# Optimization experiments

Measured on AMD Instinct MI355X. Metric: run time of the kernel, lower is better.

## Reference

```python
import jax, jax.numpy as jnp
import numpy as np

DIM_CAP = 16   # capsule dim
NCLS = 17      # annotation_nr
BS = 16
T = 120        # chunk_size * fps
P = 22         # players per frame graph
G = BS * T     # number of graphs = 1920
N = G * P      # nodes = 42240
C_IN = 14
CHS = [16, 32, 64, 152]  # 8m,16m,32m,76m with m=2
BN_EPS = 1e-3


def _build_graph():
    # fully-connected directed edges within each 22-node graph (no self loops)
    ii, jj = np.meshgrid(np.arange(P), np.arange(P), indexing='ij')
    mask = ii != jj
    li, lj = ii[mask], jj[mask]               # (462,)
    base = (np.arange(G) * P)[:, None]
    src = (base + li[None, :]).reshape(-1)
    dst = (base + lj[None, :]).reshape(-1)
    edge_index = np.stack([src, dst]).astype(np.int64)   # (2, E)
    batch = np.repeat(np.arange(G), P).astype(np.int64)  # (N,)
    return jnp.asarray(edge_index), jnp.asarray(batch)


def setup_inputs() -> dict:
    key = jax.random.key(0)
    ks = jax.random.split(key, 16)
    edge_index, batch = _build_graph()
    E = edge_index.shape[1]
    x = jax.random.normal(ks[0], (N, C_IN), dtype=jnp.float32)
    edge_attr = jax.random.uniform(ks[1], (E, 5), dtype=jnp.float32)
    dims = [C_IN] + CHS
    params = {}
    for i in range(4):
        s = 1.0 / np.sqrt(dims[i])
        params[f'W{i+1}'] = jax.random.normal(ks[2 + i], (dims[i], dims[i + 1]), dtype=jnp.float32) * s
        params[f'b{i+1}'] = jnp.zeros((dims[i + 1],), dtype=jnp.float32)
    c_out = DIM_CAP * NCLS  # 272
    params['conv_w'] = jax.random.normal(ks[6], (c_out, CHS[-1], 3), dtype=jnp.float32) * (1.0 / np.sqrt(CHS[-1] * 3))
    params['conv_b'] = jnp.zeros((c_out,), dtype=jnp.float32)
    params['bn_gamma'] = jnp.ones((T,), dtype=jnp.float32)
    params['bn_beta'] = jnp.zeros((T,), dtype=jnp.float32)
    return dict(x=x, edge_index=edge_index, batch=batch, edge_attr=edge_attr, **params)


def _gcn_layer(x, src, dst, w_edge, W, b):
    # PyG GCNConv: x' = D^-1/2 (A + I) D^-1/2 (x W) + b, edge weights w, self-loop weight 1
    n = x.shape[0]
    h = x @ W
    loop = jnp.arange(n)
    src_f = jnp.concatenate([src, loop])
    dst_f = jnp.concatenate([dst, loop])
    w_f = jnp.concatenate([w_edge, jnp.ones((n,), h.dtype)])
    deg = jax.ops.segment_sum(w_f, dst_f, num_segments=n)
    dinv = jnp.where(deg > 0, jax.lax.rsqrt(deg), 0.0)
    norm = dinv[src_f] * w_f * dinv[dst_f]
    out = jax.ops.segment_sum(norm[:, None] * h[src_f], dst_f, num_segments=n)
    return out + b


def reference(x, edge_index, batch, edge_attr, W1, b1, W2, b2, W3, b3, W4, b4,
              conv_w, conv_b, bn_gamma, bn_beta):
    src, dst = edge_index[0], edge_index[1]
    ew = edge_attr[:, 4]
    h = jax.nn.relu(_gcn_layer(x, src, dst, ew, W1, b1))
    h = jax.nn.relu(_gcn_layer(h, src, dst, ew, W2, b2))
    h = jax.nn.relu(_gcn_layer(h, src, dst, ew, W3, b3))
    h = jax.nn.relu(_gcn_layer(h, src, dst, ew, W4, b4))
    # global mean pool per graph -> (G, 152)
    ones = jnp.ones((h.shape[0],), h.dtype)
    cnt = jax.ops.segment_sum(ones, batch, num_segments=G)
    pooled = jax.ops.segment_sum(h, batch, num_segments=G) / jnp.clip(cnt, 1.0)[:, None]
    # (BS, T, 152) -> (BS, 152, T); conv kernel (3,1) with pad (1,1) on T
    feat = pooled.reshape(BS, T, CHS[-1]).transpose(0, 2, 1)
    conv = jax.lax.conv_general_dilated(
        feat, conv_w, window_strides=(1,), padding=[(1, 1)],
        dimension_numbers=('NCH', 'OIH', 'NCH'))
    conv = conv + conv_b[None, :, None]            # (BS, 272, T)
    caps = conv.transpose(0, 2, 1).reshape(BS, T, DIM_CAP, NCLS)
    # BatchNorm2d(num_features=T) in eval mode: running mean 0, var 1
    scale = (bn_gamma / jnp.sqrt(1.0 + BN_EPS))[None, :, None, None]
    shift = bn_beta[None, :, None, None]
    s = jax.nn.sigmoid(caps * scale + shift)
    out = jnp.sqrt(jnp.sum(jnp.square(s - 0.5), axis=2) * 4.0 / DIM_CAP)
    return out  # (BS, T, NCLS)
```

## Files before the change

### kernel.cpp

```cpp
#include <hip/hip_runtime.h>
#include <hip/hip_bf16.h>

#define GROUPS 1920
#define CH4 152

__device__ __forceinline__ int rh(int r) { return (r + (r >> 3)) & 7; }
__device__ __forceinline__ int swz(int r, int c) {
    return (r << 5) + ((((c >> 2) ^ rh(r)) << 2) | (c & 3));
}
__device__ __forceinline__ int swz4(int r, int c4) {
    return (r << 5) + ((c4 ^ rh(r)) << 2);
}

template<int DIN, int KR>
__device__ __forceinline__ void layerA(const float* buf, float* Ut,
                                       const float* A, int tid)
{
    constexpr int NT = (DIN / KR) * 3;
    if (tid < NT) {
        const int kt = tid / 3, pt = tid - kt * 3;
        const int p0 = pt * 8;
        float acc[KR][8];
        #pragma unroll
        for (int j = 0; j < KR; ++j)
            #pragma unroll
            for (int a = 0; a < 8; ++a) acc[j][a] = 0.f;
        #pragma unroll 2
        for (int q = 0; q < 22; ++q) {
            const float4 a0 = *(const float4*)(A + q * 28 + p0);
            const float4 a1 = *(const float4*)(A + q * 28 + p0 + 4);
            float xv[KR];
            #pragma unroll
            for (int j = 0; j < KR; ++j) xv[j] = buf[swz(kt * KR + j, q)];
            #pragma unroll
            for (int j = 0; j < KR; ++j) {
                acc[j][0] = fmaf(xv[j], a0.x, acc[j][0]);
                acc[j][1] = fmaf(xv[j], a0.y, acc[j][1]);
                acc[j][2] = fmaf(xv[j], a0.z, acc[j][2]);
                acc[j][3] = fmaf(xv[j], a0.w, acc[j][3]);
                acc[j][4] = fmaf(xv[j], a1.x, acc[j][4]);
                acc[j][5] = fmaf(xv[j], a1.y, acc[j][5]);
                acc[j][6] = fmaf(xv[j], a1.z, acc[j][6]);
                acc[j][7] = fmaf(xv[j], a1.w, acc[j][7]);
            }
        }
        #pragma unroll
        for (int j = 0; j < KR; ++j) {
            const int k = kt * KR + j;
            *(float4*)(Ut + swz4(k, pt * 2)) =
                make_float4(acc[j][0], acc[j][1], acc[j][2], acc[j][3]);
            *(float4*)(Ut + swz4(k, pt * 2 + 1)) =
                make_float4(acc[j][4], acc[j][5], acc[j][6], acc[j][7]);
        }
    }
}

template<int DIN, int DOUT, int CR>
__device__ __forceinline__ void layerB(const float* __restrict__ W,
                                       const float* __restrict__ Bb,
                                       const float* Ut, float* buf, int tid)
{
    constexpr int NT = (DOUT / CR) * 3;
    if (tid < NT) {
        const int ct = tid / 3, pt = tid - ct * 3;
        const int c0 = ct * CR;
        float acc[CR][8];
        #pragma unroll
        for (int b = 0; b < CR; ++b) {
            const float bias = Bb[c0 + b];
            #pragma unroll
            for (int a = 0; a < 8; ++a) acc[b][a] = bias;
        }
        #pragma unroll 2
        for (int k = 0; k < DIN; ++k) {
            const float4 u0 = *(const float4*)(Ut + swz4(k, pt * 2));
            const float4 u1 = *(const float4*)(Ut + swz4(k, pt * 2 + 1));
            float wv[CR];
            if constexpr (CR == 1) {
                wv[0] = W[k * DOUT + c0];
            } else if constexpr (CR == 2) {
                const float2 w2 = *(const float2*)(W + k * DOUT + c0);
                wv[0] = w2.x; wv[1] = w2.y;
            } else {
                #pragma unroll
                for (int b = 0; b < CR; b += 4) {
                    const float4 w4 = *(const float4*)(W + k * DOUT + c0 + b);
                    wv[b] = w4.x; wv[b + 1] = w4.y; wv[b + 2] = w4.z; wv[b + 3] = w4.w;
                }
            }
            #pragma unroll
            for (int b = 0; b < CR; ++b) {
                acc[b][0] = fmaf(wv[b], u0.x, acc[b][0]);
                acc[b][1] = fmaf(wv[b], u0.y, acc[b][1]);
                acc[b][2] = fmaf(wv[b], u0.z, acc[b][2]);
                acc[b][3] = fmaf(wv[b], u0.w, acc[b][3]);
                acc[b][4] = fmaf(wv[b], u1.x, acc[b][4]);
                acc[b][5] = fmaf(wv[b], u1.y, acc[b][5]);
                acc[b][6] = fmaf(wv[b], u1.z, acc[b][6]);
                acc[b][7] = fmaf(wv[b], u1.w, acc[b][7]);
            }
        }
        #pragma unroll
        for (int b = 0; b < CR; ++b) {
            const int r = c0 + b;
            *(float4*)(buf + swz4(r, pt * 2)) =
                make_float4(fmaxf(acc[b][0], 0.f), fmaxf(acc[b][1], 0.f),
                            fmaxf(acc[b][2], 0.f), fmaxf(acc[b][3], 0.f));
            *(float4*)(buf + swz4(r, pt * 2 + 1)) =
                make_float4(fmaxf(acc[b][4], 0.f), fmaxf(acc[b][5], 0.f),
                            fmaxf(acc[b][6], 0.f), fmaxf(acc[b][7], 0.f));
        }
    }
}

__global__ __launch_bounds__(64) void gcn_kernel(
    const float* __restrict__ x, const float* __restrict__ ea,
    const float* __restrict__ W1, const float* __restrict__ b1,
    const float* __restrict__ W2, const float* __restrict__ b2,
    const float* __restrict__ W3, const float* __restrict__ b3,
    const float* __restrict__ W4, const float* __restrict__ b4,
    float* __restrict__ pooledT)
{
    __shared__ __align__(16) float sA[24 * 28];
    __shared__ float dv[24];
    __shared__ __align__(16) float buf[64 * 32];
    __shared__ __align__(16) float Ut[64 * 32];

    const int tid = threadIdx.x;
    const int g = blockIdx.x;

    for (int idx = tid; idx < 24 * 28; idx += 64) {
        const int q = idx / 28, p = idx - q * 28;
        float v = 0.f;
        if (q < 22 && p < 22) {
            if (q == p) v = 1.0f;
            else {
                const int e = q * 21 + p - (p > q);
                v = ea[((size_t)g * 462 + e) * 5 + 4];
            }
        }
        sA[idx] = v;
    }
    for (int idx = tid; idx < 14 * 24; idx += 64) {
        const int k = idx / 24, p = idx - k * 24;
        buf[swz(k, p)] = (p < 22) ? x[((size_t)g * 22 + p) * 14 + k] : 0.f;
    }
    __syncthreads();

    if (tid < 24) {
        const int p = tid;
        float s = 0.f;
        #pragma unroll
        for (int q = 0; q < 22; ++q) s += sA[q * 28 + p];
        dv[p] = (s > 0.f) ? rsqrtf(s) : 0.f;
    }
    __syncthreads();
    for (int idx = tid; idx < 24 * 28; idx += 64) {
        const int q = idx / 28, p = idx - q * 28;
        if (p < 24) sA[idx] *= dv[q] * dv[p];
    }
    __syncthreads();

    layerA<14, 1>(buf, Ut, sA, tid);           __syncthreads();
    layerB<14, 16, 1>(W1, b1, Ut, buf, tid);   __syncthreads();
    layerA<16, 1>(buf, Ut, sA, tid);           __syncthreads();
    layerB<16, 32, 2>(W2, b2, Ut, buf, tid);   __syncthreads();
    layerA<32, 2>(buf, Ut, sA, tid);           __syncthreads();
    layerB<32, 64, 4>(W3, b3, Ut, buf, tid);   __syncthreads();
    layerA<64, 4>(buf, Ut, sA, tid);           __syncthreads();

    float* pscr = sA;
    if (tid < 19 * 3) {
        const int ct = tid / 3, pt = tid - ct * 3;
        const int c0 = ct * 8;
        float acc[8][8];
        #pragma unroll
        for (int b = 0; b < 8; ++b) {
            const float bias = b4[c0 + b];
            #pragma unroll
            for (int a = 0; a < 8; ++a) acc[b][a] = bias;
        }
        #pragma unroll 2
        for (int k = 0; k < 64; ++k) {
            const float4 u0 = *(const float4*)(Ut + swz4(k, pt * 2));
            const float4 u1 = *(const float4*)(Ut + swz4(k, pt * 2 + 1));
            float wv[8];
            #pragma unroll
            for (int b = 0; b < 8; b += 4) {
                const float4 w4 = *(const float4*)(W4 + k * 152 + c0 + b);
                wv[b] = w4.x; wv[b + 1] = w4.y; wv[b + 2] = w4.z; wv[b + 3] = w4.w;
            }
            #pragma unroll
            for (int b = 0; b < 8; ++b) {
                acc[b][0] = fmaf(wv[b], u0.x, acc[b][0]);
                acc[b][1] = fmaf(wv[b], u0.y, acc[b][1]);
                acc[b][2] = fmaf(wv[b], u0.z, acc[b][2]);
                acc[b][3] = fmaf(wv[b], u0.w, acc[b][3]);
                acc[b][4] = fmaf(wv[b], u1.x, acc[b][4]);
                acc[b][5] = fmaf(wv[b], u1.y, acc[b][5]);
                acc[b][6] = fmaf(wv[b], u1.z, acc[b][6]);
                acc[b][7] = fmaf(wv[b], u1.w, acc[b][7]);
            }
        }
        const int alim = (pt == 2) ? 6 : 8;
        float ps[8];
        #pragma unroll
        for (int b = 0; b < 8; ++b) {
            float s = 0.f;
            #pragma unroll
            for (int a = 0; a < 8; ++a)
                s += (a < alim) ? fmaxf(acc[b][a], 0.f) : 0.f;
            ps[b] = s;
        }
        *(float4*)(pscr + pt * 152 + c0)     = make_float4(ps[0], ps[1], ps[2], ps[3]);
        *(float4*)(pscr + pt * 152 + c0 + 4) = make_float4(ps[4], ps[5], ps[6], ps[7]);
    }
    __syncthreads();

    {
        const int b = g / 120, t = g - b * 120;
        for (int c = tid; c < 152; c += 64) {
            const float s = pscr[c] + pscr[152 + c] + pscr[304 + c];
            pooledT[(((size_t)(b * 152 + c)) << 7) + 4 + t] = s * (1.0f / 22.0f);
        }
    }
}

__global__ __launch_bounds__(256) void repack_conv_w(const float* __restrict__ cw,
                                                     float* __restrict__ wT,
                                                     float* __restrict__ pT)
{
    const int idx = blockIdx.x * 256 + threadIdx.x;
    if (idx < 272 * 456) {
        const int o = idx / 456, r = idx - o * 456;
        wT[r * 272 + o] = cw[idx];
    } else {
        const int j = idx - 272 * 456;
        if (j < 16 * 152 * 8) {
            const int row = j >> 3, s = j & 7;
            const int slot = (s < 4) ? s : s + 120;
            pT[(size_t)row * 128 + slot] = 0.f;
        }
    }
}

__global__ __launch_bounds__(320) void conv_caps_kernel(
    const float* __restrict__ pT, const float* __restrict__ wT,
    const float* __restrict__ cb, const float* __restrict__ gamma,
    const float* __restrict__ beta, float* __restrict__ out)
{
    __shared__ __align__(16) float s2[8 * 272];
    __shared__ float sc[8], sh[8];

    const int bx = blockIdx.x;
    const int b = bx / 15, tile = bx - b * 15;
    const int t0 = tile * 8;
    const int tid = threadIdx.x;

    if (tid < 8) {
        const int t = t0 + tid;
        sc[tid] = gamma[t] * 0.999500374688f;
        sh[tid] = beta[t];
    }
    __syncthreads();

    if (tid < 272) {
        const int o = tid;
        const float cb0 = cb[o];
        float acc[8];
        #pragma unroll
        for (int tt = 0; tt < 8; ++tt) acc[tt] = cb0;
        const float* wp0 = wT + o;
        const float* frow0 = pT + ((size_t)b * 152) * 128 + 3 + t0;
        float w0 = wp0[0], w1 = wp0[272], w2 = wp0[544];
        #pragma unroll 2
        for (int i = 0; i < CH4; ++i) {
            const int inext = (i == CH4 - 1) ? i : i + 1;
            const float* nwp = wp0 + inext * 816;
            const float nw0 = nwp[0], nw1 = nwp[272], nw2 = nwp[544];
            const float* f = frow0 + (size_t)i * 128;
            float fr[10];
            #pragma unroll
            for (int j = 0; j < 10; ++j) fr[j] = f[j];
            #pragma unroll
            for (int tt = 0; tt < 8; ++tt)
                acc[tt] = fmaf(w0, fr[tt], fmaf(w1, fr[tt + 1], fmaf(w2, fr[tt + 2], acc[tt])));
            w0 = nw0; w1 = nw1; w2 = nw2;
        }
        #pragma unroll
        for (int tt = 0; tt < 8; ++tt) {
            const float z = fmaf(acc[tt], sc[tt], sh[tt]);
            const float s = 1.0f / (1.0f + __expf(-z));
            const float d = s - 0.5f;
            s2[tt * 272 + o] = d * d;
        }
    }
    __syncthreads();

    for (int e = tid; e < 8 * 17; e += 320) {
        const int tt = e / 17, n = e - tt * 17;
        float s = 0.f;
        #pragma unroll
        for (int d = 0; d < 16; ++d) s += s2[tt * 272 + d * 17 + n];
        out[((size_t)b * 120 + t0 + tt) * 17 + n] = sqrtf(s) * 0.5f;
    }
}

extern "C" void kernel_launch(void* const* d_in, const int* in_sizes, int n_in,
                              void* d_out, int out_size, void* d_ws, size_t ws_size,
                              hipStream_t stream) {
    const float* x     = (const float*)d_in[0];
    const float* ea    = (const float*)d_in[3];
    const float* W1    = (const float*)d_in[4];
    const float* b1    = (const float*)d_in[5];
    const float* W2    = (const float*)d_in[6];
    const float* b2    = (const float*)d_in[7];
    const float* W3    = (const float*)d_in[8];
    const float* b3    = (const float*)d_in[9];
    const float* W4    = (const float*)d_in[10];
    const float* b4    = (const float*)d_in[11];
    const float* cw    = (const float*)d_in[12];
    const float* cb    = (const float*)d_in[13];
    const float* gamma = (const float*)d_in[14];
    const float* beta  = (const float*)d_in[15];
    float* out = (float*)d_out;

    float* pT = (float*)d_ws;
    float* wT = pT + (size_t)16 * 152 * 128;

    hipLaunchKernelGGL(repack_conv_w, dim3((272 * 456 + 16 * 152 * 8 + 255) / 256),
                       dim3(256), 0, stream, cw, wT, pT);
    hipLaunchKernelGGL(gcn_kernel, dim3(GROUPS), dim3(64), 0, stream,
                       x, ea, W1, b1, W2, b2, W3, b3, W4, b4, pT);
    hipLaunchKernelGGL(conv_caps_kernel, dim3(16 * 15), dim3(320), 0, stream,
                       pT, wT, cb, gamma, beta, out);
}
```

Measured before the change: 172.2 us.

## Double GCN block threads, halve per-thread tiles, store pooled features row-major

The GCN kernel now launches 128 threads per graph instead of 64. Register tiles in layers 2-4 are halved (CR/KR reduced, layer-4 tile goes from 8 to 4 channels) so more threads share the work, and the inner loops are unrolled 4 instead of 2. The pooled output changes from a channel-major padded layout with scattered per-channel writes to a time-major [b][t+pad][152] layout with contiguous stores. The conv kernel reads that layout with strided loads. The goal is more parallelism per graph and coalesced pooled writes, at the cost of strided feature reads in the conv kernel and more partially idle threads.

Measured after the change: 161.0 us. 6.5% less time.

```diff
diff --git a/kernel.cpp b/kernel.cpp
--- a/kernel.cpp
+++ b/kernel.cpp
@@ -71,7 +71,7 @@
             #pragma unroll
             for (int a = 0; a < 8; ++a) acc[b][a] = bias;
         }
-        #pragma unroll 2
+        #pragma unroll 4
         for (int k = 0; k < DIN; ++k) {
             const float4 u0 = *(const float4*)(Ut + swz4(k, pt * 2));
             const float4 u1 = *(const float4*)(Ut + swz4(k, pt * 2 + 1));
@@ -113,13 +113,13 @@
     }
 }
 
-__global__ __launch_bounds__(64) void gcn_kernel(
+__global__ __launch_bounds__(128, 4) void gcn_kernel(
     const float* __restrict__ x, const float* __restrict__ ea,
     const float* __restrict__ W1, const float* __restrict__ b1,
     const float* __restrict__ W2, const float* __restrict__ b2,
     const float* __restrict__ W3, const float* __restrict__ b3,
     const float* __restrict__ W4, const float* __restrict__ b4,
-    float* __restrict__ pooledT)
+    float* __restrict__ pooled)
 {
     __shared__ __align__(16) float sA[24 * 28];
     __shared__ float dv[24];
@@ -129,7 +129,7 @@
     const int tid = threadIdx.x;
     const int g = blockIdx.x;
 
-    for (int idx = tid; idx < 24 * 28; idx += 64) {
+    for (int idx = tid; idx < 24 * 28; idx += 128) {
         const int q = idx / 28, p = idx - q * 28;
         float v = 0.f;
         if (q < 22 && p < 22) {
@@ -141,7 +141,7 @@
         }
         sA[idx] = v;
     }
-    for (int idx = tid; idx < 14 * 24; idx += 64) {
+    for (int idx = tid; idx < 14 * 24; idx += 128) {
         const int k = idx / 24, p = idx - k * 24;
         buf[swz(k, p)] = (p < 22) ? x[((size_t)g * 22 + p) * 14 + k] : 0.f;
     }
@@ -155,7 +155,7 @@
         dv[p] = (s > 0.f) ? rsqrtf(s) : 0.f;
     }
     __syncthreads();
-    for (int idx = tid; idx < 24 * 28; idx += 64) {
+    for (int idx = tid; idx < 24 * 28; idx += 128) {
         const int q = idx / 28, p = idx - q * 28;
         if (p < 24) sA[idx] *= dv[q] * dv[p];
     }
@@ -164,34 +164,30 @@
     layerA<14, 1>(buf, Ut, sA, tid);           __syncthreads();
     layerB<14, 16, 1>(W1, b1, Ut, buf, tid);   __syncthreads();
     layerA<16, 1>(buf, Ut, sA, tid);           __syncthreads();
-    layerB<16, 32, 2>(W2, b2, Ut, buf, tid);   __syncthreads();
-    layerA<32, 2>(buf, Ut, sA, tid);           __syncthreads();
-    layerB<32, 64, 4>(W3, b3, Ut, buf, tid);   __syncthreads();
-    layerA<64, 4>(buf, Ut, sA, tid);           __syncthreads();
+    layerB<16, 32, 1>(W2, b2, Ut, buf, tid);   __syncthreads();
+    layerA<32, 1>(buf, Ut, sA, tid);           __syncthreads();
+    layerB<32, 64, 2>(W3, b3, Ut, buf, tid);   __syncthreads();
+    layerA<64, 2>(buf, Ut, sA, tid);           __syncthreads();
 
     float* pscr = sA;
-    if (tid < 19 * 3) {
+    if (tid < 38 * 3) {
         const int ct = tid / 3, pt = tid - ct * 3;
-        const int c0 = ct * 8;
-        float acc[8][8];
-        #pragma unroll
-        for (int b = 0; b < 8; ++b) {
+        const int c0 = ct * 4;
+        float acc[4][8];
+        #pragma unroll
+        for (int b = 0; b < 4; ++b) {
             const float bias = b4[c0 + b];
             #pragma unroll
             for (int a = 0; a < 8; ++a) acc[b][a] = bias;
         }
-        #pragma unroll 2
+        #pragma unroll 4
         for (int k = 0; k < 64; ++k) {
             const float4 u0 = *(const float4*)(Ut + swz4(k, pt * 2));
             const float4 u1 = *(const float4*)(Ut + swz4(k, pt * 2 + 1));
-            float wv[8];
-            #pragma unroll
-            for (int b = 0; b < 8; b += 4) {
-                const float4 w4 = *(const float4*)(W4 + k * 152 + c0 + b);
-                wv[b] = w4.x; wv[b + 1] = w4.y; wv[b + 2] = w4.z; wv[b + 3] = w4.w;
-            }
-            #pragma unroll
-            for (int b = 0; b < 8; ++b) {
+            const float4 w4 = *(const float4*)(W4 + k * 152 + c0);
+            const float wv[4] = {w4.x, w4.y, w4.z, w4.w};
+            #pragma unroll
+            for (int b = 0; b < 4; ++b) {
                 acc[b][0] = fmaf(wv[b], u0.x, acc[b][0]);
                 acc[b][1] = fmaf(wv[b], u0.y, acc[b][1]);
                 acc[b][2] = fmaf(wv[b], u0.z, acc[b][2]);
@@ -203,32 +199,32 @@
             }
         }
         const int alim = (pt == 2) ? 6 : 8;
-        float ps[8];
-        #pragma unroll
-        for (int b = 0; b < 8; ++b) {
+        float ps[4];
+        #pragma unroll
+        for (int b = 0; b < 4; ++b) {
             float s = 0.f;
             #pragma unroll
             for (int a = 0; a < 8; ++a)
                 s += (a < alim) ? fmaxf(acc[b][a], 0.f) : 0.f;
             ps[b] = s;
         }
-        *(float4*)(pscr + pt * 152 + c0)     = make_float4(ps[0], ps[1], ps[2], ps[3]);
-        *(float4*)(pscr + pt * 152 + c0 + 4) = make_float4(ps[4], ps[5], ps[6], ps[7]);
+        *(float4*)(pscr + pt * 152 + c0) = make_float4(ps[0], ps[1], ps[2], ps[3]);
     }
     __syncthreads();
 
     {
         const int b = g / 120, t = g - b * 120;
-        for (int c = tid; c < 152; c += 64) {
+        float* dst = pooled + ((size_t)(b * 122) + t + 1) * 152;
+        for (int c = tid; c < 152; c += 128) {
             const float s = pscr[c] + pscr[152 + c] + pscr[304 + c];
-            pooledT[(((size_t)(b * 152 + c)) << 7) + 4 + t] = s * (1.0f / 22.0f);
+            dst[c] = s * (1.0f / 22.0f);
         }
     }
 }
 
 __global__ __launch_bounds__(256) void repack_conv_w(const float* __restrict__ cw,
                                                      float* __restrict__ wT,
-                                                     float* __restrict__ pT)
+                                                     float* __restrict__ pG)
 {
     const int idx = blockIdx.x * 256 + threadIdx.x;
     if (idx < 272 * 456) {
@@ -236,16 +232,17 @@
         wT[r * 272 + o] = cw[idx];
     } else {
         const int j = idx - 272 * 456;
-        if (j < 16 * 152 * 8) {
-            const int row = j >> 3, s = j & 7;
-            const int slot = (s < 4) ? s : s + 120;
-            pT[(size_t)row * 128 + slot] = 0.f;
+        if (j < 16 * 2 * 152) {
+            const int bb = j / 304, rr = j - bb * 304;
+            const int row = (rr < 152) ? 0 : 121;
+            const int c = (rr < 152) ? rr : rr - 152;
+            pG[((size_t)bb * 122 + row) * 152 + c] = 0.f;
         }
     }
 }
 
 __global__ __launch_bounds__(320) void conv_caps_kernel(
-    const float* __restrict__ pT, const float* __restrict__ wT,
+    const float* __restrict__ pG, const float* __restrict__ wT,
     const float* __restrict__ cb, const float* __restrict__ gamma,
     const float* __restrict__ beta, float* __restrict__ out)
 {
@@ -271,17 +268,17 @@
         #pragma unroll
         for (int tt = 0; tt < 8; ++tt) acc[tt] = cb0;
         const float* wp0 = wT + o;
-        const float* frow0 = pT + ((size_t)b * 152) * 128 + 3 + t0;
+        const float* frow0 = pG + ((size_t)b * 122 + t0) * 152;
         float w0 = wp0[0], w1 = wp0[272], w2 = wp0[544];
         #pragma unroll 2
         for (int i = 0; i < CH4; ++i) {
             const int inext = (i == CH4 - 1) ? i : i + 1;
             const float* nwp = wp0 + inext * 816;
             const float nw0 = nwp[0], nw1 = nwp[272], nw2 = nwp[544];
-            const float* f = frow0 + (size_t)i * 128;
+            const float* f = frow0 + i;
             float fr[10];
             #pragma unroll
-            for (int j = 0; j < 10; ++j) fr[j] = f[j];
+            for (int j = 0; j < 10; ++j) fr[j] = f[j * 152];
             #pragma unroll
             for (int tt = 0; tt < 8; ++tt)
                 acc[tt] = fmaf(w0, fr[tt], fmaf(w1, fr[tt + 1], fmaf(w2, fr[tt + 2], acc[tt])));
@@ -325,13 +322,14 @@
     const float* beta  = (const float*)d_in[15];
     float* out = (float*)d_out;
 
-    float* pT = (float*)d_ws;
-    float* wT = pT + (size_t)16 * 152 * 128;
-
-    hipLaunchKernelGGL(repack_conv_w, dim3((272 * 456 + 16 * 152 * 8 + 255) / 256),
-                       dim3(256), 0, stream, cw, wT, pT);
-    hipLaunchKernelGGL(gcn_kernel, dim3(GROUPS), dim3(64), 0, stream,
-                       x, ea, W1, b1, W2, b2, W3, b3, W4, b4, pT);
+    float* pG = (float*)d_ws;
+    float* wT = pG + (size_t)16 * 122 * 152;
+
+    hipLaunchKernelGGL(repack_conv_w,
+                       dim3((272 * 456 + 16 * 2 * 152 + 255) / 256),
+                       dim3(256), 0, stream, cw, wT, pG);
+    hipLaunchKernelGGL(gcn_kernel, dim3(GROUPS), dim3(128), 0, stream,
+                       x, ea, W1, b1, W2, b2, W3, b3, W4, b4, pG);
     hipLaunchKernelGGL(conv_caps_kernel, dim3(16 * 15), dim3(320), 0, stream,
-                       pT, wT, cb, gamma, beta, out);
-}
+                       pG, wT, cb, gamma, beta, out);
+}
```
